# Performance work log

Measured on AMD Instinct MI355X. Metric: run time of the kernel, lower is better.

Reference implementation:

```python
import jax, jax.numpy as jnp
import numpy as np
import math

N_HEADS = 64
N_KV_HEADS = 8
HEAD_DIM = 128
DIM = 8192
SEQLEN = 2048
KVLEN = 2048
BSZ = 1


def setup_inputs() -> dict:
    key = jax.random.key(0)
    k1, k2, k3, k4, k5 = jax.random.split(key, 5)
    xq = jax.random.normal(k1, (SEQLEN, N_HEADS, BSZ, HEAD_DIM), dtype=jnp.float32)
    keys = jax.random.normal(k2, (BSZ, N_KV_HEADS, KVLEN, HEAD_DIM), dtype=jnp.float32)
    values = jax.random.normal(k3, (BSZ, N_KV_HEADS, KVLEN, HEAD_DIM), dtype=jnp.float32)
    attn_mask = jax.random.normal(k4, (SEQLEN, 1, 1, KVLEN), dtype=jnp.float32)
    wo_w = jax.random.normal(k5, (DIM, DIM), dtype=jnp.float32) * (1.0 / math.sqrt(DIM))
    return {"xq": xq, "keys": keys, "values": values, "attn_mask": attn_mask, "wo_w": wo_w}


def reference(xq, keys, values, attn_mask, wo_w):
    n_rep = N_HEADS // N_KV_HEADS
    bsz = xq.shape[2]
    seqlen = xq.shape[0]
    # repeat_kv: expand kv heads to n_heads (torch expand+reshape == jnp.repeat on head axis)
    k = jnp.repeat(keys, n_rep, axis=1)    # (b, n_heads, kv, d)
    v = jnp.repeat(values, n_rep, axis=1)  # (b, n_heads, kv, d)
    q = jnp.transpose(xq, (2, 1, 0, 3))    # (b, n_heads, s, d)
    mask = jnp.transpose(attn_mask, (2, 1, 0, 3))  # (b_or_1, h_or_1, s, kv)
    scores = jnp.einsum('bhsd,bhtd->bhst', q, k) / math.sqrt(HEAD_DIM)
    scores = scores + mask
    probs = jax.nn.softmax(scores.astype(jnp.float32), axis=-1).astype(q.dtype)
    out = jnp.einsum('bhst,bhtd->bhsd', probs, v)  # (b, h, s, d)
    out = jnp.transpose(out, (0, 2, 1, 3)).reshape(bsz, seqlen, -1)  # (b, s, h*d)
    return out @ wo_w.T  # Linear wo, no bias
```

## Files before the change

### kernel.cpp

```cpp
#include <hip/hip_runtime.h>
#include <hip/hip_bf16.h>
#include <stdint.h>


typedef __bf16 bf16;
typedef __attribute__((ext_vector_type(8))) __bf16 bf16x8;
typedef __attribute__((ext_vector_type(4))) __bf16 bf16x4;
typedef __attribute__((ext_vector_type(4))) float f32x4;
typedef __attribute__((ext_vector_type(16))) float f32x16;
typedef __attribute__((ext_vector_type(4))) unsigned int u32x4;

#define N_HEADS 64
#define N_KVH   8
#define HDIM    128
#define SEQ     2048
#define KVL     2048
#define DIM     8192

__device__ __forceinline__ void gload16(const void* g, void* l) {
  __builtin_amdgcn_global_load_lds((const __attribute__((address_space(1))) void*)g,
                                   (__attribute__((address_space(3))) void*)l,
                                   16, 0, 0);
}

__device__ __forceinline__ unsigned pack2(float lo, float hi) {
  union { bf16 h; unsigned short u; } a, b;
  a.h = (bf16)lo; b.h = (bf16)hi;
  return ((unsigned)b.u << 16) | (unsigned)a.u;
}

__device__ __forceinline__ void exch(unsigned a, unsigned b, unsigned& r0, unsigned& r1) {
  asm("v_permlane32_swap_b32 %0, %1" : "+v"(a), "+v"(b));
  r0 = a; r1 = b;
}

__device__ __forceinline__ void buildfrags(const float (&p)[16], bf16x8& f0, bf16x8& f1) {
  unsigned pk0 = pack2(p[0],  p[1]),  pk1 = pack2(p[2],  p[3]);
  unsigned pk2 = pack2(p[4],  p[5]),  pk3 = pack2(p[6],  p[7]);
  unsigned pk4 = pack2(p[8],  p[9]),  pk5 = pack2(p[10], p[11]);
  unsigned pk6 = pack2(p[12], p[13]), pk7 = pack2(p[14], p[15]);
  unsigned a0, a1, b0, b1, c0, c1, d0, d1;
  exch(pk0, pk2, a0, a1);
  exch(pk1, pk3, b0, b1);
  exch(pk4, pk6, c0, c1);
  exch(pk5, pk7, d0, d1);
  u32x4 w0 = { a0, b0, a1, b1 };
  u32x4 w1 = { c0, d0, c1, d1 };
  f0 = __builtin_bit_cast(bf16x8, w0);
  f1 = __builtin_bit_cast(bf16x8, w1);
}

__global__ void cvt_f32_bf16(const float* __restrict__ in, bf16* __restrict__ out,
                             int n4, float scale) {
  int i = blockIdx.x * blockDim.x + threadIdx.x;
  int stride = gridDim.x * blockDim.x;
  for (; i < n4; i += stride) {
    float4 v = ((const float4*)in)[i];
    bf16x4 o = { (bf16)(v.x * scale), (bf16)(v.y * scale),
                 (bf16)(v.z * scale), (bf16)(v.w * scale) };
    *(bf16x4*)(out + (long)i * 4) = o;
  }
}

__global__ void cvt_vT_kernel(const float* __restrict__ v, bf16* __restrict__ vT) {
  __shared__ bf16 tile[64][132];
  const int tid = threadIdx.x;
  const int kh = blockIdx.x >> 5;
  const int t0 = (blockIdx.x & 31) << 6;
  const float* src = v + ((long)kh * KVL + t0) * HDIM;
#pragma unroll
  for (int it = 0; it < 8; ++it) {
    int q = it * 256 + tid;
    int r = q >> 5;
    int c4 = (q & 31) << 2;
    float4 val = *(const float4*)(src + (long)r * HDIM + c4);
    bf16x4 o = { (bf16)val.x, (bf16)val.y, (bf16)val.z, (bf16)val.w };
    *(bf16x4*)&tile[r][c4] = o;
  }
  __syncthreads();
  const int t = tid & 63;
  const int dbase = tid >> 6;
#pragma unroll
  for (int it = 0; it < 32; ++it) {
    int d = it * 4 + dbase;
    vT[((long)kh * HDIM + d) * KVL + t0 + t] = tile[t][d];
  }
}

__global__ __launch_bounds__(512, 2) void attn_kernel(
    const bf16* __restrict__ qB, const bf16* __restrict__ kB,
    const bf16* __restrict__ vT, const float* __restrict__ mask,
    bf16* __restrict__ attnB)
{
  __shared__ __align__(16) char lds[65536];

  const int tid  = threadIdx.x;
  const int lane = tid & 63;
  const int w    = tid >> 6;
  const int ihi  = lane >> 5;
  const int l31  = lane & 31;

  const int bid = blockIdx.x;
  const int h   = bid >> 3;
  const int q0b = (bid & 7) << 8;
  const int kh  = h >> 3;

#pragma unroll
  for (int rnd = 0; rnd < 8; ++rnd) {
    int row = rnd * 32 + w * 4 + (lane >> 4);
    int cg  = (lane & 15) ^ (row & 15);
    const bf16* g = qB + (((long)(q0b + row) * N_HEADS + h) << 7) + (cg << 3);
    gload16(g, lds + rnd * 8192 + w * 1024);
  }
  __syncthreads();

  bf16x8 qf[8];
  {
    int qrow = (w << 5) + l31;
    const char* qr = lds + qrow * 256;
#pragma unroll
    for (int s = 0; s < 8; ++s)
      qf[s] = *(const bf16x8*)(qr + ((((s << 1) | ihi) ^ (qrow & 15)) << 4));
  }
  __syncthreads();

  {
#pragma unroll
    for (int rnd = 0; rnd < 2; ++rnd) {
      int row = rnd * 32 + w * 4 + (lane >> 4);
      int cg  = (lane & 15) ^ (row & 15);
      const bf16* g = kB + (((long)(kh * KVL + row)) << 7) + (cg << 3);
      gload16(g, lds + rnd * 8192 + w * 1024);
    }
#pragma unroll
    for (int rnd = 0; rnd < 2; ++rnd) {
      int vr = rnd * 32 + w * 4 + (lane >> 4);
      int gg = (lane & 15) ^ (vr & 15);
      int dsrc = (vr << 1) | (gg >> 3);
      const bf16* gp = vT + ((long)(kh * HDIM + dsrc) * KVL) + ((gg & 7) << 3);
      gload16(gp, lds + 32768 + rnd * 8192 + w * 1024);
    }
  }
  __syncthreads();

  const float* mrow = mask + (size_t)(q0b + (w << 5) + l31) * KVL + (ihi << 2);

  f32x16 acc[4];
#pragma unroll
  for (int dt = 0; dt < 4; ++dt) acc[dt] = {};
  float m_run = -1e30f, l_run = 0.f;

  for (int kt = 0; kt < KVL / 64; ++kt) {
    const int cur = kt & 1;
    const int kv0 = kt << 6;

    if (kt < KVL / 64 - 1) {
      const int kv0n = kv0 + 64;
#pragma unroll
      for (int rnd = 0; rnd < 2; ++rnd) {
        int row = rnd * 32 + w * 4 + (lane >> 4);
        int cg  = (lane & 15) ^ (row & 15);
        const bf16* g = kB + (((long)(kh * KVL + kv0n + row)) << 7) + (cg << 3);
        gload16(g, lds + (cur ^ 1) * 16384 + rnd * 8192 + w * 1024);
      }
#pragma unroll
      for (int rnd = 0; rnd < 2; ++rnd) {
        int vr = rnd * 32 + w * 4 + (lane >> 4);
        int gg = (lane & 15) ^ (vr & 15);
        int dsrc = (vr << 1) | (gg >> 3);
        const bf16* gp = vT + ((long)(kh * HDIM + dsrc) * KVL) + kv0n + ((gg & 7) << 3);
        gload16(gp, lds + 32768 + (cur ^ 1) * 16384 + rnd * 8192 + w * 1024);
      }
    }

    const float* mrt = mrow + kv0;
    f32x4 mk0[4], mk1[4];
#pragma unroll
    for (int rq = 0; rq < 4; ++rq) {
      mk0[rq] = *(const f32x4*)(mrt + (rq << 3));
      mk1[rq] = *(const f32x4*)(mrt + 32 + (rq << 3));
    }

    const char* kb = lds + cur * 16384;
    f32x16 s0 = {}, s1 = {};
    const int kr0 = l31, kr1 = 32 + l31;
    __builtin_amdgcn_s_setprio(1);
#pragma unroll
    for (int s = 0; s < 8; ++s) {
      bf16x8 kf0 = *(const bf16x8*)(kb + kr0 * 256 + ((((s << 1) | ihi) ^ (kr0 & 15)) << 4));
      s0 = __builtin_amdgcn_mfma_f32_32x32x16_bf16(kf0, qf[s], s0, 0, 0, 0);
      bf16x8 kf1 = *(const bf16x8*)(kb + kr1 * 256 + ((((s << 1) | ihi) ^ (kr1 & 15)) << 4));
      s1 = __builtin_amdgcn_mfma_f32_32x32x16_bf16(kf1, qf[s], s1, 0, 0, 0);
    }
    __builtin_amdgcn_s_setprio(0);

    float p0[16], p1[16];
#pragma unroll
    for (int rq = 0; rq < 4; ++rq) {
#pragma unroll
      for (int j = 0; j < 4; ++j) {
        p0[rq * 4 + j] = s0[rq * 4 + j] + mk0[rq][j];
        p1[rq * 4 + j] = s1[rq * 4 + j] + mk1[rq][j];
      }
    }

    float q00 = fmaxf(fmaxf(p0[0],  p0[1]),  fmaxf(p0[2],  p0[3]));
    float q01 = fmaxf(fmaxf(p0[4],  p0[5]),  fmaxf(p0[6],  p0[7]));
    float q02 = fmaxf(fmaxf(p0[8],  p0[9]),  fmaxf(p0[10], p0[11]));
    float q03 = fmaxf(fmaxf(p0[12], p0[13]), fmaxf(p0[14], p0[15]));
    float q10 = fmaxf(fmaxf(p1[0],  p1[1]),  fmaxf(p1[2],  p1[3]));
    float q11 = fmaxf(fmaxf(p1[4],  p1[5]),  fmaxf(p1[6],  p1[7]));
    float q12 = fmaxf(fmaxf(p1[8],  p1[9]),  fmaxf(p1[10], p1[11]));
    float q13 = fmaxf(fmaxf(p1[12], p1[13]), fmaxf(p1[14], p1[15]));
    float mx = fmaxf(fmaxf(fmaxf(q00, q01), fmaxf(q02, q03)),
                     fmaxf(fmaxf(q10, q11), fmaxf(q12, q13)));
    mx = fmaxf(mx, __shfl_xor(mx, 32));
    if (!__all((int)(mx - m_run <= 8.0f))) {
      float nm = fmaxf(m_run, mx);
      float al = __expf(m_run - nm);
      m_run = nm;
      l_run *= al;
#pragma unroll
      for (int dt = 0; dt < 4; ++dt) acc[dt] *= al;
    }
    float ps = 0.f;
#pragma unroll
    for (int i = 0; i < 16; ++i) { p0[i] = __expf(p0[i] - m_run); ps += p0[i]; }
#pragma unroll
    for (int i = 0; i < 16; ++i) { p1[i] = __expf(p1[i] - m_run); ps += p1[i]; }
    ps += __shfl_xor(ps, 32);
    l_run += ps;

    bf16x8 pfrag[4];
    buildfrags(p0, pfrag[0], pfrag[1]);
    buildfrags(p1, pfrag[2], pfrag[3]);

    const char* vb = lds + 32768 + cur * 16384;
    const int par8 = (l31 & 1) << 3;
    __builtin_amdgcn_s_setprio(1);
#pragma unroll
    for (int dt = 0; dt < 4; ++dt) {
      const int vrow = (dt << 4) + (l31 >> 1);
      const char* vrp = vb + vrow * 256;
#pragma unroll
      for (int ks = 0; ks < 4; ++ks) {
        int c16 = par8 | (ks << 1) | ihi;
        bf16x8 vf = *(const bf16x8*)(vrp + ((c16 ^ (vrow & 15)) << 4));
        acc[dt] = __builtin_amdgcn_mfma_f32_32x32x16_bf16(vf, pfrag[ks], acc[dt], 0, 0, 0);
      }
    }
    __builtin_amdgcn_s_setprio(0);
    __syncthreads();
  }

  const float linv = 1.0f / l_run;
  char* ep = lds + (w << 13);
#pragma unroll
  for (int dt = 0; dt < 4; ++dt) {
#pragma unroll
    for (int r = 0; r < 16; ++r) {
      int d = (dt << 5) + (r & 3) + ((r >> 2) << 3) + (ihi << 2);
      int byte = l31 * 256 + (((d >> 3) ^ (l31 & 15)) << 4) + ((d & 7) << 1);
      *(bf16*)(ep + byte) = (bf16)(acc[dt][r] * linv);
    }
  }
  __syncthreads();
  const size_t obase = (size_t)(q0b + (w << 5)) * DIM + h * HDIM;
#pragma unroll
  for (int i = 0; i < 8; ++i) {
    int row = (i << 2) + (lane >> 4);
    int cp  = lane & 15;
    int c   = cp ^ (row & 15);
    bf16x8 ov = *(const bf16x8*)(ep + row * 256 + (cp << 4));
    *(bf16x8*)(attnB + obase + (size_t)row * DIM + (c << 3)) = ov;
  }
}

__global__ __launch_bounds__(512, 2) void gemm_bt(
    const bf16* __restrict__ A, const bf16* __restrict__ B, float* __restrict__ C)
{
  __shared__ __align__(16) char lds[131072];
  const int tid  = threadIdx.x;
  const int lane = tid & 63;
  const int w    = tid >> 6;
  const int wm   = w >> 2;
  const int wn   = w & 3;

  const int bid = blockIdx.x;
  const int m0  = (bid >> 5) << 8;
  const int n0  = (((bid & 7) << 2) | ((bid >> 3) & 3)) << 8;

  const int srow = tid >> 3;
  const int sch  = (tid & 7) ^ (srow & 7);
  const bf16* gA0 = A + (long)(m0 + srow) * DIM + (sch << 3);
  const bf16* gB0 = B + (long)(n0 + srow) * DIM + (sch << 3);
  const long rstep = (long)64 * DIM;

  f32x4 acc[8][4];
#pragma unroll
  for (int i = 0; i < 8; ++i)
#pragma unroll
    for (int j = 0; j < 4; ++j) acc[i][j] = { 0.f, 0.f, 0.f, 0.f };

  auto STAGE = [&](int kt) {
    const long ko = (long)kt << 6;
    char* s = lds + (kt & 1) * 65536 + tid * 16;
#pragma unroll
    for (int l = 0; l < 4; ++l)
      gload16(gA0 + l * rstep + ko, s + l * 8192);
#pragma unroll
    for (int l = 0; l < 4; ++l)
      gload16(gB0 + l * rstep + ko, s + 32768 + l * 8192);
  };

  const int g = lane >> 4;
  const int l15 = lane & 15;
  auto COMPUTE = [&](int buf) {
    const char* ab = lds + buf * 65536;
    const char* bb = ab + 32768;
    bf16x8 bfr[4][2];
#pragma unroll
    for (int j = 0; j < 4; ++j) {
      int n = (wn << 6) + (j << 4) + l15;
      const char* nr = bb + n * 128;
#pragma unroll
      for (int ks = 0; ks < 2; ++ks)
        bfr[j][ks] = *(const bf16x8*)(nr + ((((ks << 2) | g) ^ (n & 7)) << 4));
    }
#pragma unroll
    for (int p = 0; p < 4; ++p) {
      bf16x8 af[2][2];
#pragma unroll
      for (int e = 0; e < 2; ++e) {
        int m = (wm << 7) + (((p << 1) | e) << 4) + l15;
        const char* mr = ab + m * 128;
#pragma unroll
        for (int ks = 0; ks < 2; ++ks)
          af[e][ks] = *(const bf16x8*)(mr + ((((ks << 2) | g) ^ (m & 7)) << 4));
      }
      __builtin_amdgcn_s_setprio(1);
#pragma unroll
      for (int e = 0; e < 2; ++e)
#pragma unroll
        for (int j = 0; j < 4; ++j)
#pragma unroll
          for (int ks = 0; ks < 2; ++ks)
            acc[(p << 1) | e][j] =
              __builtin_amdgcn_mfma_f32_16x16x32_bf16(af[e][ks], bfr[j][ks],
                                                      acc[(p << 1) | e][j], 0, 0, 0);
      __builtin_amdgcn_s_setprio(0);
    }
  };

  STAGE(0);
  STAGE(1);

  for (int t = 0; t < 126; ++t) {
    asm volatile("s_waitcnt vmcnt(8)" ::: "memory");
    __builtin_amdgcn_s_barrier();
    COMPUTE(t & 1);
    __builtin_amdgcn_s_barrier();
    STAGE(t + 2);
  }
  asm volatile("s_waitcnt vmcnt(8)" ::: "memory");
  __builtin_amdgcn_s_barrier();
  COMPUTE(0);
  asm volatile("s_waitcnt vmcnt(0)" ::: "memory");
  __builtin_amdgcn_s_barrier();
  COMPUTE(1);

#pragma unroll
  for (int i = 0; i < 8; ++i) {
#pragma unroll
    for (int rr = 0; rr < 4; ++rr) {
      float* cp = C + (long)(m0 + (wm << 7) + (i << 4) + ((lane >> 4) << 2) + rr) * DIM
                    + n0 + (wn << 6) + l15;
#pragma unroll
      for (int j = 0; j < 4; ++j)
        cp[j * 16] = acc[i][j][rr];
    }
  }
}

extern "C" void kernel_launch(void* const* d_in, const int* in_sizes, int n_in,
                              void* d_out, int out_size, void* d_ws, size_t ws_size,
                              hipStream_t stream) {
  const float* xq     = (const float*)d_in[0];
  const float* keys   = (const float*)d_in[1];
  const float* values = (const float*)d_in[2];
  const float* mask   = (const float*)d_in[3];
  const float* wo     = (const float*)d_in[4];
  float* out = (float*)d_out;
  char* ws = (char*)d_ws;

  bf16* woB = (bf16*)ws;
  bf16* qB  = (bf16*)(ws + 134217728ull);
  bf16* kB  = (bf16*)(ws + 134217728ull + 33554432ull);
  bf16* vT  = (bf16*)(ws + 134217728ull + 37748736ull);
  bf16* aB  = (bf16*)(ws + 134217728ull + 41943040ull);

  cvt_f32_bf16<<<dim3(2048), dim3(256), 0, stream>>>(wo, woB, 16777216, 1.0f);
  cvt_f32_bf16<<<dim3(1024), dim3(256), 0, stream>>>(xq, qB, 4194304, 0.08838834764831845f);
  cvt_f32_bf16<<<dim3(256),  dim3(256), 0, stream>>>(keys, kB, 524288, 1.0f);
  cvt_vT_kernel<<<dim3(256), dim3(256), 0, stream>>>(values, vT);
  attn_kernel<<<dim3(512),   dim3(512), 0, stream>>>(qB, kB, vT, mask, aB);
  gemm_bt<<<dim3(256),       dim3(512), 0, stream>>>(aB, woB, out);
}
```

Before: 552.1 us.

## Use exp2 softmax with log2e-folded scale and restructure GEMM into quarter-phase pipeline

The attention softmax now works in base 2: the Q scale absorbs log2(e), the mask is added with an FMA times log2(e), and exp2f replaces __expf, with the rescale threshold adjusted to match. The output-projection GEMM drops its two-tile-ahead staging with vmcnt(8) and instead interleaves the next tile's global-to-LDS loads in four quarters between MFMA phases, with a barrier between each quarter. Fragment reads are split into smaller A/B groups to lower register pressure. The risk is less prefetch distance, since the GEMM waits on vmcnt(0) every iteration, plus more barriers.

```diff
diff --git a/kernel.cpp b/kernel.cpp
--- a/kernel.cpp
+++ b/kernel.cpp
@@ -16,6 +16,7 @@
 #define SEQ     2048
 #define KVL     2048
 #define DIM     8192
+#define LOG2E   1.4426950408889634f
 
 __device__ __forceinline__ void gload16(const void* g, void* l) {
   __builtin_amdgcn_global_load_lds((const __attribute__((address_space(1))) void*)g,
@@ -199,8 +200,8 @@
     for (int rq = 0; rq < 4; ++rq) {
 #pragma unroll
       for (int j = 0; j < 4; ++j) {
-        p0[rq * 4 + j] = s0[rq * 4 + j] + mk0[rq][j];
-        p1[rq * 4 + j] = s1[rq * 4 + j] + mk1[rq][j];
+        p0[rq * 4 + j] = fmaf(mk0[rq][j], LOG2E, s0[rq * 4 + j]);
+        p1[rq * 4 + j] = fmaf(mk1[rq][j], LOG2E, s1[rq * 4 + j]);
       }
     }
 
@@ -215,9 +216,9 @@
     float mx = fmaxf(fmaxf(fmaxf(q00, q01), fmaxf(q02, q03)),
                      fmaxf(fmaxf(q10, q11), fmaxf(q12, q13)));
     mx = fmaxf(mx, __shfl_xor(mx, 32));
-    if (!__all((int)(mx - m_run <= 8.0f))) {
+    if (!__all((int)(mx - m_run <= 11.5415603f))) {
       float nm = fmaxf(m_run, mx);
-      float al = __expf(m_run - nm);
+      float al = exp2f(m_run - nm);
       m_run = nm;
       l_run *= al;
 #pragma unroll
@@ -225,9 +226,9 @@
     }
     float ps = 0.f;
 #pragma unroll
-    for (int i = 0; i < 16; ++i) { p0[i] = __expf(p0[i] - m_run); ps += p0[i]; }
-#pragma unroll
-    for (int i = 0; i < 16; ++i) { p1[i] = __expf(p1[i] - m_run); ps += p1[i]; }
+    for (int i = 0; i < 16; ++i) { p0[i] = exp2f(p0[i] - m_run); ps += p0[i]; }
+#pragma unroll
+    for (int i = 0; i < 16; ++i) { p1[i] = exp2f(p1[i] - m_run); ps += p1[i]; }
     ps += __shfl_xor(ps, 32);
     l_run += ps;
 
@@ -302,72 +303,102 @@
 #pragma unroll
     for (int j = 0; j < 4; ++j) acc[i][j] = { 0.f, 0.f, 0.f, 0.f };
 
-  auto STAGE = [&](int kt) {
+  const int g = lane >> 4;
+  const int l15 = lane & 15;
+
+  bf16x8 af[4][2];
+  bf16x8 bfr[2][2];
+
+  auto STAGE_A2 = [&](int kt, int hh) {
     const long ko = (long)kt << 6;
     char* s = lds + (kt & 1) * 65536 + tid * 16;
-#pragma unroll
-    for (int l = 0; l < 4; ++l)
-      gload16(gA0 + l * rstep + ko, s + l * 8192);
-#pragma unroll
-    for (int l = 0; l < 4; ++l)
-      gload16(gB0 + l * rstep + ko, s + 32768 + l * 8192);
+    gload16(gA0 + (2 * hh) * rstep + ko, s + (2 * hh) * 8192);
+    gload16(gA0 + (2 * hh + 1) * rstep + ko, s + (2 * hh + 1) * 8192);
   };
-
-  const int g = lane >> 4;
-  const int l15 = lane & 15;
-  auto COMPUTE = [&](int buf) {
-    const char* ab = lds + buf * 65536;
+  auto STAGE_B2 = [&](int kt, int hh) {
+    const long ko = (long)kt << 6;
+    char* s = lds + (kt & 1) * 65536 + 32768 + tid * 16;
+    gload16(gB0 + (2 * hh) * rstep + ko, s + (2 * hh) * 8192);
+    gload16(gB0 + (2 * hh + 1) * rstep + ko, s + (2 * hh + 1) * 8192);
+  };
+  auto RD_AF = [&](const char* ab, int mg) {
+#pragma unroll
+    for (int i = 0; i < 4; ++i) {
+      int m = (wm << 7) + (mg << 6) + (i << 4) + l15;
+      const char* mr = ab + m * 128;
+      af[i][0] = *(const bf16x8*)(mr + ((g ^ (m & 7)) << 4));
+      af[i][1] = *(const bf16x8*)(mr + (((4 | g) ^ (m & 7)) << 4));
+    }
+  };
+  auto RD_BF = [&](const char* bb, int nh) {
+#pragma unroll
+    for (int j = 0; j < 2; ++j) {
+      int n = (wn << 6) + (nh << 5) + (j << 4) + l15;
+      const char* nr = bb + n * 128;
+      bfr[j][0] = *(const bf16x8*)(nr + ((g ^ (n & 7)) << 4));
+      bfr[j][1] = *(const bf16x8*)(nr + (((4 | g) ^ (n & 7)) << 4));
+    }
+  };
+  auto MM = [&](int mg, int nh) {
+    __builtin_amdgcn_s_setprio(1);
+#pragma unroll
+    for (int i = 0; i < 4; ++i)
+#pragma unroll
+      for (int j = 0; j < 2; ++j)
+#pragma unroll
+        for (int ks = 0; ks < 2; ++ks)
+          acc[(mg << 2) | i][(nh << 1) | j] =
+            __builtin_amdgcn_mfma_f32_16x16x32_bf16(af[i][ks], bfr[j][ks],
+                                                    acc[(mg << 2) | i][(nh << 1) | j], 0, 0, 0);
+    __builtin_amdgcn_s_setprio(0);
+  };
+
+  STAGE_A2(0, 0);
+  STAGE_A2(0, 1);
+  STAGE_B2(0, 0);
+  STAGE_B2(0, 1);
+
+  for (int t = 0; t < 127; ++t) {
+    const char* ab = lds + (t & 1) * 65536;
     const char* bb = ab + 32768;
-    bf16x8 bfr[4][2];
-#pragma unroll
-    for (int j = 0; j < 4; ++j) {
-      int n = (wn << 6) + (j << 4) + l15;
-      const char* nr = bb + n * 128;
-#pragma unroll
-      for (int ks = 0; ks < 2; ++ks)
-        bfr[j][ks] = *(const bf16x8*)(nr + ((((ks << 2) | g) ^ (n & 7)) << 4));
-    }
-#pragma unroll
-    for (int p = 0; p < 4; ++p) {
-      bf16x8 af[2][2];
-#pragma unroll
-      for (int e = 0; e < 2; ++e) {
-        int m = (wm << 7) + (((p << 1) | e) << 4) + l15;
-        const char* mr = ab + m * 128;
-#pragma unroll
-        for (int ks = 0; ks < 2; ++ks)
-          af[e][ks] = *(const bf16x8*)(mr + ((((ks << 2) | g) ^ (m & 7)) << 4));
-      }
-      __builtin_amdgcn_s_setprio(1);
-#pragma unroll
-      for (int e = 0; e < 2; ++e)
-#pragma unroll
-        for (int j = 0; j < 4; ++j)
-#pragma unroll
-          for (int ks = 0; ks < 2; ++ks)
-            acc[(p << 1) | e][j] =
-              __builtin_amdgcn_mfma_f32_16x16x32_bf16(af[e][ks], bfr[j][ks],
-                                                      acc[(p << 1) | e][j], 0, 0, 0);
-      __builtin_amdgcn_s_setprio(0);
-    }
-  };
-
-  STAGE(0);
-  STAGE(1);
-
-  for (int t = 0; t < 126; ++t) {
-    asm volatile("s_waitcnt vmcnt(8)" ::: "memory");
+    asm volatile("s_waitcnt vmcnt(0)" ::: "memory");
     __builtin_amdgcn_s_barrier();
-    COMPUTE(t & 1);
+    asm volatile("" ::: "memory");
+    RD_AF(ab, 0);
+    RD_BF(bb, 0);
+    STAGE_A2(t + 1, 0);
+    MM(0, 0);
     __builtin_amdgcn_s_barrier();
-    STAGE(t + 2);
-  }
-  asm volatile("s_waitcnt vmcnt(8)" ::: "memory");
-  __builtin_amdgcn_s_barrier();
-  COMPUTE(0);
-  asm volatile("s_waitcnt vmcnt(0)" ::: "memory");
-  __builtin_amdgcn_s_barrier();
-  COMPUTE(1);
+    RD_BF(bb, 1);
+    STAGE_A2(t + 1, 1);
+    MM(0, 1);
+    __builtin_amdgcn_s_barrier();
+    RD_AF(ab, 1);
+    RD_BF(bb, 0);
+    STAGE_B2(t + 1, 0);
+    MM(1, 0);
+    __builtin_amdgcn_s_barrier();
+    RD_BF(bb, 1);
+    STAGE_B2(t + 1, 1);
+    MM(1, 1);
+  }
+  {
+    const char* ab = lds + 65536;
+    const char* bb = ab + 32768;
+    asm volatile("s_waitcnt vmcnt(0)" ::: "memory");
+    __builtin_amdgcn_s_barrier();
+    asm volatile("" ::: "memory");
+    RD_AF(ab, 0);
+    RD_BF(bb, 0);
+    MM(0, 0);
+    RD_BF(bb, 1);
+    MM(0, 1);
+    RD_AF(ab, 1);
+    RD_BF(bb, 0);
+    MM(1, 0);
+    RD_BF(bb, 1);
+    MM(1, 1);
+  }
 
 #pragma unroll
   for (int i = 0; i < 8; ++i) {
@@ -400,7 +431,7 @@
   bf16* aB  = (bf16*)(ws + 134217728ull + 41943040ull);
 
   cvt_f32_bf16<<<dim3(2048), dim3(256), 0, stream>>>(wo, woB, 16777216, 1.0f);
-  cvt_f32_bf16<<<dim3(1024), dim3(256), 0, stream>>>(xq, qB, 4194304, 0.08838834764831845f);
+  cvt_f32_bf16<<<dim3(1024), dim3(256), 0, stream>>>(xq, qB, 4194304, 0.1275174403f);
   cvt_f32_bf16<<<dim3(256),  dim3(256), 0, stream>>>(keys, kB, 524288, 1.0f);
   cvt_vT_kernel<<<dim3(256), dim3(256), 0, stream>>>(values, vT);
   attn_kernel<<<dim3(512),   dim3(512), 0, stream>>>(qB, kB, vT, mask, aB);
```

New measurement: 590.5 us. 1.07x slower.

## Load GEMM B operand directly from global into registers, bypassing LDS

Applied to the files above, without the earlier changes.

The output-projection GEMM now stages only the A tile through LDS and reads B fragments straight from global memory into registers inside the compute step. This halves LDS use per block to 64 KB, which may let a second block fit on each CU, and the wait count is adjusted to the smaller number of LDS loads in flight. In exchange, B global-load latency sits directly in front of the MFMAs with no prefetch. B is also re-read by both wave rows instead of being shared through LDS, and the compiler's waits on the B loads may drain the A prefetch as well.

```diff
diff --git a/kernel.cpp b/kernel.cpp
--- a/kernel.cpp
+++ b/kernel.cpp
@@ -279,7 +279,7 @@
 __global__ __launch_bounds__(512, 2) void gemm_bt(
     const bf16* __restrict__ A, const bf16* __restrict__ B, float* __restrict__ C)
 {
-  __shared__ __align__(16) char lds[131072];
+  __shared__ __align__(16) char lds[65536];
   const int tid  = threadIdx.x;
   const int lane = tid & 63;
   const int w    = tid >> 6;
@@ -293,40 +293,37 @@
   const int srow = tid >> 3;
   const int sch  = (tid & 7) ^ (srow & 7);
   const bf16* gA0 = A + (long)(m0 + srow) * DIM + (sch << 3);
-  const bf16* gB0 = B + (long)(n0 + srow) * DIM + (sch << 3);
   const long rstep = (long)64 * DIM;
 
+  const int g = lane >> 4;
+  const int l15 = lane & 15;
+
+  const bf16* gBn = B + (long)(n0 + (wn << 6) + l15) * DIM + (g << 3);
+  const long jstep = (long)16 * DIM;
+
   f32x4 acc[8][4];
 #pragma unroll
   for (int i = 0; i < 8; ++i)
 #pragma unroll
     for (int j = 0; j < 4; ++j) acc[i][j] = { 0.f, 0.f, 0.f, 0.f };
 
-  auto STAGE = [&](int kt) {
+  auto STAGE_A = [&](int kt) {
     const long ko = (long)kt << 6;
-    char* s = lds + (kt & 1) * 65536 + tid * 16;
+    char* s = lds + (kt & 1) * 32768 + tid * 16;
 #pragma unroll
     for (int l = 0; l < 4; ++l)
       gload16(gA0 + l * rstep + ko, s + l * 8192);
-#pragma unroll
-    for (int l = 0; l < 4; ++l)
-      gload16(gB0 + l * rstep + ko, s + 32768 + l * 8192);
   };
 
-  const int g = lane >> 4;
-  const int l15 = lane & 15;
-  auto COMPUTE = [&](int buf) {
-    const char* ab = lds + buf * 65536;
-    const char* bb = ab + 32768;
+  auto COMPUTE = [&](int buf, int kt) {
+    const char* ab = lds + buf * 32768;
+    const long k0 = (long)kt << 6;
     bf16x8 bfr[4][2];
 #pragma unroll
-    for (int j = 0; j < 4; ++j) {
-      int n = (wn << 6) + (j << 4) + l15;
-      const char* nr = bb + n * 128;
+    for (int j = 0; j < 4; ++j)
 #pragma unroll
       for (int ks = 0; ks < 2; ++ks)
-        bfr[j][ks] = *(const bf16x8*)(nr + ((((ks << 2) | g) ^ (n & 7)) << 4));
-    }
+        bfr[j][ks] = *(const bf16x8*)(gBn + (long)j * jstep + k0 + (ks << 5));
 #pragma unroll
     for (int p = 0; p < 4; ++p) {
       bf16x8 af[2][2];
@@ -352,22 +349,22 @@
     }
   };
 
-  STAGE(0);
-  STAGE(1);
+  STAGE_A(0);
+  STAGE_A(1);
 
   for (int t = 0; t < 126; ++t) {
-    asm volatile("s_waitcnt vmcnt(8)" ::: "memory");
+    asm volatile("s_waitcnt vmcnt(4)" ::: "memory");
     __builtin_amdgcn_s_barrier();
-    COMPUTE(t & 1);
+    COMPUTE(t & 1, t);
     __builtin_amdgcn_s_barrier();
-    STAGE(t + 2);
-  }
-  asm volatile("s_waitcnt vmcnt(8)" ::: "memory");
+    STAGE_A(t + 2);
+  }
+  asm volatile("s_waitcnt vmcnt(4)" ::: "memory");
   __builtin_amdgcn_s_barrier();
-  COMPUTE(0);
+  COMPUTE(0, 126);
   asm volatile("s_waitcnt vmcnt(0)" ::: "memory");
   __builtin_amdgcn_s_barrier();
-  COMPUTE(1);
+  COMPUTE(1, 127);
 
 #pragma unroll
   for (int i = 0; i < 8; ++i) {
```

Result: slower. 735.3 us (+33.2%).
